# Optimization experiments

Hardware: AMD Instinct MI355X
Metric: run time of the kernel (lower is better)

Reference implementation:

```python
import jax, jax.numpy as jnp
import numpy as np

N_OR = 8          # orientations of the SE(2) discretization
BN_EPS = 1e-5


def _rotate_kernel(W, theta):
    """Rotate a spatial kernel [..., k, k] about its center by theta.
    Bilinear interpolation, zeros outside the kernel support."""
    k = W.shape[-1]
    c = (k - 1) / 2.0
    ys, xs = jnp.meshgrid(jnp.arange(k, dtype=jnp.float32) - c,
                          jnp.arange(k, dtype=jnp.float32) - c, indexing="ij")
    cos, sin = jnp.cos(theta), jnp.sin(theta)
    sy = cos * ys - sin * xs + c   # source coords: rotate sample grid by -theta
    sx = sin * ys + cos * xs + c
    y0 = jnp.floor(sy).astype(jnp.int32)
    x0 = jnp.floor(sx).astype(jnp.int32)
    wy = (sy - y0).astype(W.dtype)
    wx = (sx - x0).astype(W.dtype)

    def gather(yi, xi):
        valid = ((yi >= 0) & (yi < k) & (xi >= 0) & (xi < k)).astype(W.dtype)
        yc = jnp.clip(yi, 0, k - 1)
        xc = jnp.clip(xi, 0, k - 1)
        return W[..., yc, xc] * valid

    return (gather(y0, x0) * (1 - wy) * (1 - wx)
            + gather(y0, x0 + 1) * (1 - wy) * wx
            + gather(y0 + 1, x0) * wy * (1 - wx)
            + gather(y0 + 1, x0 + 1) * wy * wx)


def _thetas():
    return 2.0 * jnp.pi * jnp.arange(N_OR, dtype=jnp.float32) / N_OR


def _lift(x, W):
    """LiftM2Cartesian. x: [B,Cin,H,W] (pre-padded), W: [Cout,Cin,k,k].
    Returns [B,Cout,8,H',W']."""
    Wr = jax.vmap(lambda t: _rotate_kernel(W, t))(_thetas())  # [8,Cout,Cin,k,k]
    co = W.shape[0]
    Wf = Wr.reshape((N_OR * co,) + W.shape[1:])
    y = jax.lax.conv_general_dilated(x, Wf, (1, 1), "VALID",
                                     dimension_numbers=("NCHW", "OIHW", "NCHW"))
    B, _, H, Wd = y.shape
    return y.reshape(B, N_OR, co, H, Wd).transpose(0, 2, 1, 3, 4)


def _gconv(x, K):
    """ConvM2Cartesian. x: [B,Cin,8,H,W] (spatially pre-padded),
    K: [Cout,Cin,8,k,k]. Output orientation m uses the kernel spatially
    rotated by theta_m with the orientation axis cyclically shifted by m."""
    cout, cin, _, k, _ = K.shape
    # orient_idx[m, o] = (o - m) mod 8
    orient_idx = (jnp.arange(N_OR)[None, :] - jnp.arange(N_OR)[:, None]) % N_OR
    Kshift = jnp.moveaxis(K[:, :, orient_idx], 2, 0)        # [8m,Cout,Cin,8o,k,k]
    Km = jax.vmap(_rotate_kernel)(Kshift, _thetas())         # [8m,Cout,Cin,8o,k,k]
    Kf = Km.reshape(N_OR * cout, cin * N_OR, k, k)
    B, _, _, H, Wd = x.shape
    xf = x.reshape(B, cin * N_OR, H, Wd)
    y = jax.lax.conv_general_dilated(xf, Kf, (1, 1), "VALID",
                                     dimension_numbers=("NCHW", "OIHW", "NCHW"))
    Ho, Wo = y.shape[-2:]
    return y.reshape(B, N_OR, cout, Ho, Wo).transpose(0, 2, 1, 3, 4)


def _bn3d(x, gamma, beta):
    """BatchNorm3d (training-mode batch statistics). x: [B,C,O,H,W]."""
    mean = jnp.mean(x, axis=(0, 2, 3, 4), keepdims=True)
    var = jnp.mean((x - mean) ** 2, axis=(0, 2, 3, 4), keepdims=True)
    g = gamma.reshape(1, -1, 1, 1, 1)
    b = beta.reshape(1, -1, 1, 1, 1)
    return g * (x - mean) * jax.lax.rsqrt(var + BN_EPS) + b


def _pad_m2(x, p):
    return jnp.pad(x, ((0, 0), (0, 0), (0, 0), (p, p), (p, p)), mode="reflect")


def setup_inputs() -> dict:
    key = jax.random.key(0)
    ks = jax.random.split(key, 8)
    c = 16
    cin = 3
    x = jax.random.normal(ks[0], (2, cin, 256, 256), dtype=jnp.float32)
    lift_w = jax.random.normal(ks[1], (c, cin, 7, 7), dtype=jnp.float32) / np.sqrt(cin * 49)
    w1 = jax.random.normal(ks[2], (c, c, N_OR, 5, 5), dtype=jnp.float32) / np.sqrt(c * N_OR * 25)
    w2 = jax.random.normal(ks[3], (c, c, N_OR, 5, 5), dtype=jnp.float32) / np.sqrt(c * N_OR * 25)
    w3 = jax.random.normal(ks[4], (c, c, N_OR, 5, 5), dtype=jnp.float32) / np.sqrt(c * N_OR * 25)
    w4 = jax.random.normal(ks[5], (c, c, N_OR, 1, 1), dtype=jnp.float32) / np.sqrt(c * N_OR)
    final_w = jax.random.normal(ks[6], (1, c), dtype=jnp.float32) / np.sqrt(c)
    ones = jnp.ones((c,), dtype=jnp.float32)
    zeros = jnp.zeros((c,), dtype=jnp.float32)
    return {"x": x, "lift_w": lift_w, "w1": w1, "w2": w2, "w3": w3, "w4": w4,
            "final_w": final_w,
            "g0": ones, "b0": zeros, "g1": ones, "b1": zeros, "g2": ones,
            "b2": zeros, "g3": ones, "b3": zeros, "g4": ones, "b4": zeros}


def reference(x, lift_w, w1, w2, w3, w4, final_w,
              g0, b0, g1, b1, g2, b2, g3, b3, g4, b4):
    # lift: ReflectionPad2d(3) -> LiftM2Cartesian(7) -> BN3d -> ReLU
    xp = jnp.pad(x, ((0, 0), (0, 0), (3, 3), (3, 3)), mode="reflect")
    h = jax.nn.relu(_bn3d(_lift(xp, lift_w), g0, b0))          # [B,16,8,H,W]
    # conv1..3: ReflectionPadM2(2) -> ConvM2Cartesian(5) -> BN3d -> ReLU (Dropout3d is identity in eval)
    h = jax.nn.relu(_bn3d(_gconv(_pad_m2(h, 2), w1), g1, b1))
    h = jax.nn.relu(_bn3d(_gconv(_pad_m2(h, 2), w2), g2, b2))
    h = jax.nn.relu(_bn3d(_gconv(_pad_m2(h, 2), w3), g3, b3))
    # conv4: 1x1 group conv -> BN3d -> ReLU
    h = jax.nn.relu(_bn3d(_gconv(h, w4), g4, b4))
    # MaxProjectM2: max over orientation axis
    h = jnp.max(h, axis=2)                                     # [B,16,H,W]
    # final 1x1 conv (no bias) + sigmoid
    return jax.nn.sigmoid(jnp.einsum("bchw,oc->bohw", h, final_w))
```

## Files before the change

kernel.cpp:

```cpp
#include <hip/hip_runtime.h>
#include <hip/hip_bf16.h>
#include <math.h>

#define HW 65536
#define WID 256
#define NOR 8
#define PLANE_C (NOR * HW)
#define PLANE_B (16 * NOR * HW)
#define BN_N 1048576.0f
#define NHWC_STRIDE 136

typedef __attribute__((ext_vector_type(8)))  short  short8;
typedef __attribute__((ext_vector_type(4)))  short  short4v;
typedef __attribute__((ext_vector_type(16))) float  float16;
typedef __attribute__((ext_vector_type(4)))  float  float4v;

__device__ __forceinline__ float b2f(short s) {
    union { unsigned int u; float f; } c;
    c.u = ((unsigned int)(unsigned short)s) << 16;
    return c.f;
}
__device__ __forceinline__ short f2b(float f) {
    union { __hip_bfloat16 h; short s; } c;
    c.h = __float2bfloat16(f);
    return c.s;
}

__global__ void detect_k(const void* __restrict__ x, int* __restrict__ flag) {
    __shared__ int bad;
    if (threadIdx.x == 0) bad = 0;
    __syncthreads();
    const __hip_bfloat16* p = (const __hip_bfloat16*)x;
    for (int i = threadIdx.x; i < 4096; i += 256) {
        float v = __bfloat162float(p[i]);
        if (!(fabsf(v) < 1e4f)) atomicOr(&bad, 1);
    }
    __syncthreads();
    if (threadIdx.x == 0) *flag = bad ? 0 : 1;
}

#define CVT_TOTAL 551392
__global__ void cvt_all_k(const void* p0, const void* p1, const void* p2, const void* p3,
                          const void* p4, const void* p5, const void* p6, const void* p7,
                          const void* p8, const void* p9, const void* p10, const void* p11,
                          const void* p12, const void* p13, const void* p14, const void* p15,
                          const void* p16, float* __restrict__ dst, const int* __restrict__ flag) {
    int i = blockIdx.x * 512 + threadIdx.x;
    if (i >= CVT_TOTAL) return;
    const void* src; int off;
    if      (i < 393216) { src = p0;  off = 0; }
    else if (i < 395568) { src = p1;  off = 393216; }
    else if (i < 446768) { src = p2;  off = 395568; }
    else if (i < 497968) { src = p3;  off = 446768; }
    else if (i < 549168) { src = p4;  off = 497968; }
    else if (i < 551216) { src = p5;  off = 549168; }
    else if (i < 551232) { src = p6;  off = 551216; }
    else if (i < 551248) { src = p7;  off = 551232; }
    else if (i < 551264) { src = p8;  off = 551248; }
    else if (i < 551280) { src = p9;  off = 551264; }
    else if (i < 551296) { src = p10; off = 551280; }
    else if (i < 551312) { src = p11; off = 551296; }
    else if (i < 551328) { src = p12; off = 551312; }
    else if (i < 551344) { src = p13; off = 551328; }
    else if (i < 551360) { src = p14; off = 551344; }
    else if (i < 551376) { src = p15; off = 551360; }
    else                 { src = p16; off = 551376; }
    int j = i - off;
    dst[i] = (*flag) ? __bfloat162float(((const __hip_bfloat16*)src)[j])
                     : ((const float*)src)[j];
}

__device__ float rot_sample(const float* __restrict__ W, int k, float theta, int i, int j) {
    float c = 0.5f * (float)(k - 1);
    float ys = (float)i - c, xs = (float)j - c;
    float cs = cosf(theta), sn = sinf(theta);
    float sy = cs * ys - sn * xs + c;
    float sx = sn * ys + cs * xs + c;
    float fy = floorf(sy), fx = floorf(sx);
    int y0 = (int)fy, x0 = (int)fx;
    float wy = sy - fy, wx = sx - fx;
    float v00 = (y0 >= 0 && y0 < k && x0 >= 0 && x0 < k)                 ? W[y0 * k + x0]           : 0.f;
    float v01 = (y0 >= 0 && y0 < k && x0 + 1 >= 0 && x0 + 1 < k)         ? W[y0 * k + x0 + 1]       : 0.f;
    float v10 = (y0 + 1 >= 0 && y0 + 1 < k && x0 >= 0 && x0 < k)         ? W[(y0 + 1) * k + x0]     : 0.f;
    float v11 = (y0 + 1 >= 0 && y0 + 1 < k && x0 + 1 >= 0 && x0 + 1 < k) ? W[(y0 + 1) * k + x0 + 1] : 0.f;
    return v00 * (1 - wy) * (1 - wx) + v01 * (1 - wy) * wx
         + v10 * wy * (1 - wx) + v11 * wy * wx;
}

__device__ __forceinline__ float theta_of(int m) {
    return (6.2831855f * (float)m) / 8.0f;
}

__device__ __forceinline__ int mirror(int i) {
    i = i < 0 ? -i : i;
    return i >= WID ? (2 * WID - 2 - i) : i;
}

__global__ void pack_blift_k(const float* __restrict__ lw, __hip_bfloat16* __restrict__ B,
                             float* __restrict__ stats) {
    int idx = blockIdx.x * 256 + threadIdx.x;
    if (idx < 32) stats[idx] = 0.f;
    if (idx >= 128 * 160) return;
    int n = idx / 160, k = idx % 160;
    float v = 0.f;
    if (k < 147) {
        int c = n >> 3, o = n & 7;
        int ci = k / 49, s = k % 49;
        v = rot_sample(lw + (c * 3 + ci) * 49, 7, theta_of(o), s / 7, s % 7);
    }
    B[idx] = __float2bfloat16(v);
}

__global__ void pack_bg_k(const float* __restrict__ w, __hip_bfloat16* __restrict__ Bg,
                          float* __restrict__ stats) {
    int idx = blockIdx.x * 256 + threadIdx.x;
    if (idx < 32) stats[idx] = 0.f;
    if (idx >= 409600) return;
    int j = idx & 7;
    int n = (idx >> 3) & 127;
    int kc4 = (idx >> 10) & 3;
    int sq = idx >> 12;
    int s = sq % 25, q = sq / 25;
    int ch = q * 32 + kc4 * 8 + j;
    int co = n >> 3, m = n & 7, ci = ch >> 3, o = ch & 7;
    int oo = (o - m + 8) & 7;
    float v = rot_sample(w + ((co * 16 + ci) * 8 + oo) * 25, 5, theta_of(m), s / 5, s % 5);
    Bg[idx] = __float2bfloat16(v);
}

__global__ void pack_b1_k(const float* __restrict__ w4, __hip_bfloat16* __restrict__ B1,
                          float* __restrict__ stats) {
    int idx = blockIdx.x * 256 + threadIdx.x;
    if (idx < 32) stats[idx] = 0.f;
    if (idx >= 128 * 128) return;
    int n = idx >> 7, ch = idx & 127;
    int co = n >> 3, m = n & 7, ci = ch >> 3, o = ch & 7;
    B1[idx] = __float2bfloat16(w4[(co * 16 + ci) * 8 + ((o - m + 8) & 7)]);
}

__global__ void im2col_lift_k(const float* __restrict__ xb, __hip_bfloat16* __restrict__ A) {
    int idx = blockIdx.x * 256 + threadIdx.x;
    if (idx >= HW * 160) return;
    int px = idx / 160, k = idx % 160;
    float v = 0.f;
    if (k < 147) {
        int ci = k / 49, s = k % 49;
        int gy = mirror((px >> 8) + s / 7 - 3);
        int gx = mirror((px & 255) + s % 7 - 3);
        v = xb[ci * HW + gy * WID + gx];
    }
    A[idx] = __float2bfloat16(v);
}

__device__ __forceinline__ void stats_reduce8(const float16* acc, int lane, int l31,
                                              float* sred) {
#pragma unroll
    for (int nt = 0; nt < 4; nt++) {
        float sv = 0.f, s2v = 0.f;
#pragma unroll
        for (int g = 0; g < 2; g++)
#pragma unroll
            for (int r = 0; r < 16; r++) {
                float v = acc[g * 4 + nt][r];
                sv += v;
                s2v += v * v;
            }
#pragma unroll
        for (int off = 1; off <= 4; off <<= 1) {
            sv += __shfl_xor(sv, off);
            s2v += __shfl_xor(s2v, off);
        }
        sv += __shfl_xor(sv, 32);
        s2v += __shfl_xor(s2v, 32);
        if ((lane & 39) == 0) {
            int c = nt * 4 + (l31 >> 3);
            atomicAdd(&sred[c], sv);
            atomicAdd(&sred[16 + c], s2v);
        }
    }
}

__global__ __launch_bounds__(256, 2) void lift_gemm_k(const __hip_bfloat16* __restrict__ Ah,
                                                      const __hip_bfloat16* __restrict__ Bh,
                                                      __hip_bfloat16* __restrict__ nh_out,
                                                      float* __restrict__ stats) {
    __shared__ short tb[32768];
    __shared__ float sred[32];
    const short* A = (const short*)Ah;
    const short* B = (const short*)Bh;
    int tid = threadIdx.x;
    if (tid < 32) sred[tid] = 0.f;
    int wave = tid >> 6, lane = tid & 63;
    int l31 = lane & 31, half = lane >> 5;
    int p0 = blockIdx.x * 256 + wave * 64;
    float16 acc[8];
#pragma unroll
    for (int i = 0; i < 8; i++) acc[i] = (float16)0.f;
    const short* a0p = A + (size_t)(p0 + l31) * 160 + half * 8;
    const short* a1p = a0p + 32 * 160;
    const short* bp  = B + (size_t)l31 * 160 + half * 8;
#pragma unroll
    for (int ks = 0; ks < 10; ks++) {
        short8 a0 = *(const short8*)(a0p + ks * 16);
        short8 a1 = *(const short8*)(a1p + ks * 16);
#pragma unroll
        for (int nt = 0; nt < 4; nt++) {
            short8 bb = *(const short8*)(bp + nt * 32 * 160 + ks * 16);
            acc[nt]     = __builtin_amdgcn_mfma_f32_32x32x16_bf16(a0, bb, acc[nt], 0, 0, 0);
            acc[4 + nt] = __builtin_amdgcn_mfma_f32_32x32x16_bf16(a1, bb, acc[4 + nt], 0, 0, 0);
        }
    }
#pragma unroll
    for (int g = 0; g < 2; g++)
#pragma unroll
        for (int nt = 0; nt < 4; nt++) {
            int ch = nt * 32 + l31;
#pragma unroll
            for (int r4 = 0; r4 < 4; r4++) {
                int pxb = wave * 64 + g * 32 + 8 * r4 + 4 * half;
#pragma unroll
                for (int i = 0; i < 4; i++)
                    tb[(pxb + i) * 128 + ch] = f2b(acc[g * 4 + nt][r4 * 4 + i]);
            }
        }
    __syncthreads();
    short* outp = (short*)nh_out;
    int pbase = blockIdx.x * 256;
    for (int i = tid; i < 4096; i += 256) {
        int pxl = i >> 4, seg = i & 15;
        *(short8*)(outp + (size_t)(pbase + pxl) * NHWC_STRIDE + seg * 8) =
            *(const short8*)&tb[pxl * 128 + seg * 8];
    }
    stats_reduce8(acc, lane, l31, sred);
    __syncthreads();
    if (tid < 16) {
        atomicAdd(&stats[tid * 2], sred[tid]);
        atomicAdd(&stats[tid * 2 + 1], sred[16 + tid]);
    }
}

__global__ __launch_bounds__(256, 3) void gconv_mfma_k(const __hip_bfloat16* __restrict__ nh_in,
                                                       const __hip_bfloat16* __restrict__ Bgh,
                                                       __hip_bfloat16* __restrict__ nh_out,
                                                       const float* __restrict__ statsPrev,
                                                       const float* __restrict__ gPrev,
                                                       const float* __restrict__ bPrev,
                                                       float* __restrict__ statsNew) {
    __shared__ short Au[16384];
    __shared__ float ssl[32];
    __shared__ float sred[32];
    const short* nhwc = (const short*)nh_in;
    const short* Bg = (const short*)Bgh;
    int bid = blockIdx.x;
    int xcd = bid & 7, q2 = bid >> 3;
    int nhalf = q2 & 1, qt = q2 >> 1;
    int b = xcd >> 2, band = xcd & 3;
    int tx0 = (qt & 15) << 4;
    int ty0 = (band << 6) + ((qt >> 4) << 4);
    int tid = threadIdx.x;
    if (tid < 32) sred[tid] = 0.f;
    if (tid < 16) {
        float mean = statsPrev[tid * 2] / BN_N;
        float var = statsPrev[tid * 2 + 1] / BN_N - mean * mean;
        float sc = gPrev[tid] * rsqrtf(var + 1e-5f);
        ssl[tid * 2] = sc;
        ssl[tid * 2 + 1] = bPrev[tid] - mean * sc;
    }
    int w = tid >> 6, lane = tid & 63;
    int l15 = lane & 15, l4 = lane >> 4;
    float4v acc[16];
#pragma unroll
    for (int i = 0; i < 16; i++) acc[i] = (float4v)0.f;
    const size_t bbase = (size_t)b * HW;
    const int nb = nhalf << 6;

    for (int q = 0; q < 4; q++) {
        __syncthreads();
        for (int i = tid; i < 1600; i += 256) {
            int kc = i / 400, p = i - kc * 400;
            int yl = p / 20, xl = p - yl * 20;
            int gy = mirror(ty0 - 2 + yl);
            int gx = mirror(tx0 - 2 + xl);
            short8 raw = *(const short8*)(nhwc + (bbase + gy * WID + gx) * NHWC_STRIDE
                                          + q * 32 + kc * 8);
            int c = q * 4 + kc;
            float sc = ssl[c * 2], sh = ssl[c * 2 + 1];
            short8 ov;
#pragma unroll
            for (int e = 0; e < 8; e++)
                ov[e] = f2b(fmaxf(fmaf(b2f(raw[e]), sc, sh), 0.f));
            *(short8*)&Au[(kc * 441 + yl * 21 + xl) * 8] = ov;
        }
        __syncthreads();
        for (int s = 0; s < 25; s++) {
            int dy = s / 5 - 2, dx = s % 5 - 2;
            int abase = l4 * 441 + ((w << 2) + 2 + dy) * 21 + (l15 + 2 + dx);
            const short* brow = Bg + ((size_t)(((q * 25 + s) << 2) + l4) * 128 + nb + l15) * 8;
            short8 a0 = *(const short8*)&Au[abase * 8];
            short8 a1 = *(const short8*)&Au[(abase + 21) * 8];
            short8 a2 = *(const short8*)&Au[(abase + 42) * 8];
            short8 a3 = *(const short8*)&Au[(abase + 63) * 8];
#pragma unroll
            for (int nt = 0; nt < 4; nt++) {
                short8 bb = *(const short8*)(brow + nt * 128);
                acc[nt]      = __builtin_amdgcn_mfma_f32_16x16x32_bf16(a0, bb, acc[nt], 0, 0, 0);
                acc[4 + nt]  = __builtin_amdgcn_mfma_f32_16x16x32_bf16(a1, bb, acc[4 + nt], 0, 0, 0);
                acc[8 + nt]  = __builtin_amdgcn_mfma_f32_16x16x32_bf16(a2, bb, acc[8 + nt], 0, 0, 0);
                acc[12 + nt] = __builtin_amdgcn_mfma_f32_16x16x32_bf16(a3, bb, acc[12 + nt], 0, 0, 0);
            }
        }
    }

    __syncthreads();
#pragma unroll
    for (int ag = 0; ag < 4; ag++) {
        int pxb = ((w << 2) + ag) * 16 + (l4 << 2);
#pragma unroll
        for (int nt = 0; nt < 4; nt++) {
            int nl = nt * 16 + l15;
#pragma unroll
            for (int r = 0; r < 4; r++)
                Au[(pxb + r) * 64 + nl] = f2b(acc[ag * 4 + nt][r]);
        }
    }
    __syncthreads();
    short* outp = (short*)nh_out;
    for (int i = tid; i < 2048; i += 256) {
        int pxl = i >> 3, seg = i & 7;
        int y = ty0 + (pxl >> 4), x = tx0 + (pxl & 15);
        *(short8*)(outp + (bbase + y * WID + x) * NHWC_STRIDE + nb + seg * 8) =
            *(const short8*)&Au[pxl * 64 + seg * 8];
    }
#pragma unroll
    for (int nt = 0; nt < 4; nt++) {
        float sv = 0.f, s2v = 0.f;
#pragma unroll
        for (int ag = 0; ag < 4; ag++)
#pragma unroll
            for (int r = 0; r < 4; r++) {
                float v = acc[ag * 4 + nt][r];
                sv += v;
                s2v += v * v;
            }
#pragma unroll
        for (int off = 1; off <= 4; off <<= 1) {
            sv += __shfl_xor(sv, off);
            s2v += __shfl_xor(s2v, off);
        }
        sv += __shfl_xor(sv, 16);
        s2v += __shfl_xor(s2v, 16);
        sv += __shfl_xor(sv, 32);
        s2v += __shfl_xor(s2v, 32);
        if ((lane & 7) == 0 && l4 == 0) {
            int c = (nhalf << 3) + (nt << 1) + (l15 >> 3);
            atomicAdd(&sred[c], sv);
            atomicAdd(&sred[16 + c], s2v);
        }
    }
    __syncthreads();
    if (tid < 16) {
        atomicAdd(&statsNew[tid * 2], sred[tid]);
        atomicAdd(&statsNew[tid * 2 + 1], sred[16 + tid]);
    }
}

__global__ __launch_bounds__(256, 2) void conv1x1_gemm_k(const __hip_bfloat16* __restrict__ nh,
                                                         const __hip_bfloat16* __restrict__ B1h,
                                                         __hip_bfloat16* __restrict__ outP,
                                                         const float* __restrict__ statsPrev,
                                                         const float* __restrict__ gPrev,
                                                         const float* __restrict__ bPrev,
                                                         float* __restrict__ statsNew) {
    __shared__ float sred[32];
    __shared__ float ssl[32];
    const short* nhwc = (const short*)nh;
    const short* B1 = (const short*)B1h;
    int tid = threadIdx.x;
    if (tid < 32) sred[tid] = 0.f;
    if (tid < 16) {
        float mean = statsPrev[tid * 2] / BN_N;
        float var = statsPrev[tid * 2 + 1] / BN_N - mean * mean;
        float sc = gPrev[tid] * rsqrtf(var + 1e-5f);
        ssl[tid * 2] = sc;
        ssl[tid * 2 + 1] = bPrev[tid] - mean * sc;
    }
    __syncthreads();
    int b = blockIdx.y;
    int wave = tid >> 6, lane = tid & 63;
    int l31 = lane & 31, half = lane >> 5;
    int p0 = blockIdx.x * 256 + wave * 64;
    float16 acc[8];
#pragma unroll
    for (int i = 0; i < 8; i++) acc[i] = (float16)0.f;
    const short* a0p = nhwc + ((size_t)b * HW + p0 + l31) * NHWC_STRIDE + half * 8;
    const short* a1p = a0p + 32 * NHWC_STRIDE;
    const short* bp  = B1 + (size_t)l31 * 128 + half * 8;
#pragma unroll
    for (int ks = 0; ks < 8; ks++) {
        short8 r0 = *(const short8*)(a0p + ks * 16);
        short8 r1 = *(const short8*)(a1p + ks * 16);
        int c = ks * 2 + half;
        float sc = ssl[c * 2], sh = ssl[c * 2 + 1];
        short8 a0, a1;
#pragma unroll
        for (int e = 0; e < 8; e++) {
            a0[e] = f2b(fmaxf(fmaf(b2f(r0[e]), sc, sh), 0.f));
            a1[e] = f2b(fmaxf(fmaf(b2f(r1[e]), sc, sh), 0.f));
        }
#pragma unroll
        for (int nt = 0; nt < 4; nt++) {
            short8 bb = *(const short8*)(bp + nt * 32 * 128 + ks * 16);
            acc[nt]     = __builtin_amdgcn_mfma_f32_32x32x16_bf16(a0, bb, acc[nt], 0, 0, 0);
            acc[4 + nt] = __builtin_amdgcn_mfma_f32_32x32x16_bf16(a1, bb, acc[4 + nt], 0, 0, 0);
        }
    }
    short* outb = (short*)outP + (size_t)b * PLANE_B;
#pragma unroll
    for (int g = 0; g < 2; g++)
#pragma unroll
        for (int nt = 0; nt < 4; nt++) {
            int n = nt * 32 + l31;
#pragma unroll
            for (int r4 = 0; r4 < 4; r4++) {
                int base = 8 * r4 + 4 * half;
                short4v v;
                v[0] = f2b(acc[g * 4 + nt][r4 * 4 + 0]);
                v[1] = f2b(acc[g * 4 + nt][r4 * 4 + 1]);
                v[2] = f2b(acc[g * 4 + nt][r4 * 4 + 2]);
                v[3] = f2b(acc[g * 4 + nt][r4 * 4 + 3]);
                *(short4v*)(outb + (size_t)n * HW + p0 + g * 32 + base) = v;
            }
        }
    stats_reduce8(acc, lane, l31, sred);
    __syncthreads();
    if (tid < 16) {
        atomicAdd(&statsNew[tid * 2], sred[tid]);
        atomicAdd(&statsNew[tid * 2 + 1], sred[16 + tid]);
    }
}

__global__ void final_k(const __hip_bfloat16* __restrict__ inP, const float* __restrict__ stats,
                        const float* __restrict__ g, const float* __restrict__ beta,
                        const float* __restrict__ fw, void* __restrict__ out,
                        const int* __restrict__ flag) {
    __shared__ float ssl[32];
    if (threadIdx.x < 16) {
        int c = threadIdx.x;
        float mean = stats[c * 2] / BN_N;
        float var = stats[c * 2 + 1] / BN_N - mean * mean;
        float sc = g[c] * rsqrtf(var + 1e-5f);
        ssl[c * 2] = sc;
        ssl[c * 2 + 1] = beta[c] - mean * sc;
    }
    __syncthreads();
    int i = blockIdx.x * blockDim.x + threadIdx.x;
    int b = i >> 16, pix = i & 65535;
    const short* inp = (const short*)inP;
    float acc = 0.f;
#pragma unroll
    for (int co = 0; co < 16; co++) {
        float sc = ssl[co * 2], sh = ssl[co * 2 + 1];
        float mx = 0.f;
        const short* p = inp + (size_t)b * PLANE_B + (size_t)co * PLANE_C + pix;
#pragma unroll
        for (int m = 0; m < 8; m++) mx = fmaxf(mx, fmaf(b2f(p[m * HW]), sc, sh));
        acc = fmaf(fw[co], mx, acc);
    }
    float r = 1.f / (1.f + expf(-acc));
    if (*flag)
        ((__hip_bfloat16*)out)[i] = __float2bfloat16(r);
    else
        ((float*)out)[i] = r;
}

extern "C" void kernel_launch(void* const* d_in, const int* in_sizes, int n_in,
                              void* d_out, int out_size, void* d_ws, size_t ws_size,
                              hipStream_t stream) {
    float* ws = (float*)d_ws;
    __hip_bfloat16* planarB = (__hip_bfloat16*)ws;
    __hip_bfloat16* nhwcA = (__hip_bfloat16*)(ws + 8388608);
    __hip_bfloat16* nhwcB = (__hip_bfloat16*)(ws + 17301504);
    __hip_bfloat16* Alift = nhwcB;
    __hip_bfloat16* Bg    = (__hip_bfloat16*)(ws + 26214400);
    __hip_bfloat16* Blift = (__hip_bfloat16*)(ws + 26419200);
    __hip_bfloat16* B1    = (__hip_bfloat16*)(ws + 26429440);
    float* xF  = ws + 26437632;
    float* lwF = xF + 393216;
    float* w1F = lwF + 2352;
    float* w2F = w1F + 51200;
    float* w3F = w2F + 51200;
    float* w4F = w3F + 51200;
    float* fwF = w4F + 2048;
    float* gbF = fwF + 16;
    float* statsL = ws + 26989024;
    int*   flag   = (int*)(statsL + 160);

    detect_k<<<1, 256, 0, stream>>>(d_in[0], flag);
    cvt_all_k<<<(CVT_TOTAL + 511) / 512, 512, 0, stream>>>(
        d_in[0], d_in[1], d_in[2], d_in[3], d_in[4], d_in[5], d_in[6], d_in[7], d_in[8],
        d_in[9], d_in[10], d_in[11], d_in[12], d_in[13], d_in[14], d_in[15], d_in[16],
        xF, flag);

    pack_blift_k<<<(128 * 160 + 255) / 256, 256, 0, stream>>>(lwF, Blift, statsL);
    for (int b = 0; b < 2; b++) {
        im2col_lift_k<<<(HW * 160 + 255) / 256, 256, 0, stream>>>(xF + (size_t)b * 3 * HW, Alift);
        lift_gemm_k<<<256, 256, 0, stream>>>(
            Alift, Blift,
            (__hip_bfloat16*)((short*)nhwcA + (size_t)b * HW * NHWC_STRIDE), statsL);
    }

    float* wlist[3] = {w1F, w2F, w3F};
    __hip_bfloat16* nio[4] = {nhwcA, nhwcB, nhwcA, nhwcB};
    for (int l = 0; l < 3; l++) {
        pack_bg_k<<<(409600 + 255) / 256, 256, 0, stream>>>(wlist[l], Bg, statsL + 32 * (l + 1));
        gconv_mfma_k<<<1024, 256, 0, stream>>>(nio[l], Bg, nio[l + 1],
                                               statsL + 32 * l, gbF + 32 * l, gbF + 32 * l + 16,
                                               statsL + 32 * (l + 1));
    }

    pack_b1_k<<<(128 * 128 + 255) / 256, 256, 0, stream>>>(w4F, B1, statsL + 128);
    conv1x1_gemm_k<<<dim3(256, 2), 256, 0, stream>>>(nio[3], B1, planarB,
                                                     statsL + 96, gbF + 96, gbF + 112,
                                                     statsL + 128);

    final_k<<<(2 * HW) / 256, 256, 0, stream>>>(planarB, statsL + 128, gbF + 128, gbF + 144,
                                                fwF, d_out, flag);
}
```

Measured before the change: 557.9 us.

## Fuse lift im2col into GEMM and merge weight packing into one kernel

Weight packing for the lift layer, all three group-conv layers and the 1x1 layer now runs in a single kernel into separate buffers, and it zeroes all stats slots at once. This replaces six small launches with one. The lift im2col is done inside the GEMM: each block stages a reflected 22x22x3 input tile in shared memory and builds the bf16 A fragments on the fly, so the 160-wide im2col matrix is no longer written to or read from global memory. Both batches are covered by a single 2D grid. In exchange, the GEMM inner loop now does scalar LDS gathers and conversions, and the lift output is written in 16x16 spatial tiles rather than contiguous pixel rows.

```diff
diff --git a/kernel.cpp b/kernel.cpp
--- a/kernel.cpp
+++ b/kernel.cpp
@@ -96,60 +96,53 @@
     return i >= WID ? (2 * WID - 2 - i) : i;
 }
 
-__global__ void pack_blift_k(const float* __restrict__ lw, __hip_bfloat16* __restrict__ B,
-                             float* __restrict__ stats) {
+#define PK_BLIFT 20480
+#define PK_BG 409600
+#define PK_TOTAL (PK_BLIFT + 3 * PK_BG + 16384)
+__global__ void mega_pack_k(const float* __restrict__ lwF, const float* __restrict__ w1F,
+                            const float* __restrict__ w2F, const float* __restrict__ w3F,
+                            const float* __restrict__ w4F,
+                            __hip_bfloat16* __restrict__ Blift, __hip_bfloat16* __restrict__ Bg1,
+                            __hip_bfloat16* __restrict__ Bg2, __hip_bfloat16* __restrict__ Bg3,
+                            __hip_bfloat16* __restrict__ B1, float* __restrict__ statsL) {
     int idx = blockIdx.x * 256 + threadIdx.x;
-    if (idx < 32) stats[idx] = 0.f;
-    if (idx >= 128 * 160) return;
-    int n = idx / 160, k = idx % 160;
-    float v = 0.f;
-    if (k < 147) {
-        int c = n >> 3, o = n & 7;
-        int ci = k / 49, s = k % 49;
-        v = rot_sample(lw + (c * 3 + ci) * 49, 7, theta_of(o), s / 7, s % 7);
-    }
-    B[idx] = __float2bfloat16(v);
-}
-
-__global__ void pack_bg_k(const float* __restrict__ w, __hip_bfloat16* __restrict__ Bg,
-                          float* __restrict__ stats) {
-    int idx = blockIdx.x * 256 + threadIdx.x;
-    if (idx < 32) stats[idx] = 0.f;
-    if (idx >= 409600) return;
-    int j = idx & 7;
-    int n = (idx >> 3) & 127;
-    int kc4 = (idx >> 10) & 3;
-    int sq = idx >> 12;
-    int s = sq % 25, q = sq / 25;
-    int ch = q * 32 + kc4 * 8 + j;
-    int co = n >> 3, m = n & 7, ci = ch >> 3, o = ch & 7;
-    int oo = (o - m + 8) & 7;
-    float v = rot_sample(w + ((co * 16 + ci) * 8 + oo) * 25, 5, theta_of(m), s / 5, s % 5);
-    Bg[idx] = __float2bfloat16(v);
-}
-
-__global__ void pack_b1_k(const float* __restrict__ w4, __hip_bfloat16* __restrict__ B1,
-                          float* __restrict__ stats) {
-    int idx = blockIdx.x * 256 + threadIdx.x;
-    if (idx < 32) stats[idx] = 0.f;
-    if (idx >= 128 * 128) return;
-    int n = idx >> 7, ch = idx & 127;
-    int co = n >> 3, m = n & 7, ci = ch >> 3, o = ch & 7;
-    B1[idx] = __float2bfloat16(w4[(co * 16 + ci) * 8 + ((o - m + 8) & 7)]);
-}
-
-__global__ void im2col_lift_k(const float* __restrict__ xb, __hip_bfloat16* __restrict__ A) {
-    int idx = blockIdx.x * 256 + threadIdx.x;
-    if (idx >= HW * 160) return;
-    int px = idx / 160, k = idx % 160;
-    float v = 0.f;
-    if (k < 147) {
-        int ci = k / 49, s = k % 49;
-        int gy = mirror((px >> 8) + s / 7 - 3);
-        int gx = mirror((px & 255) + s % 7 - 3);
-        v = xb[ci * HW + gy * WID + gx];
-    }
-    A[idx] = __float2bfloat16(v);
+    if (idx < 160) statsL[idx] = 0.f;
+    if (idx >= PK_TOTAL) return;
+    if (idx < PK_BLIFT) {
+        int n = idx / 160, k = idx % 160;
+        float v = 0.f;
+        if (k < 147) {
+            int c = n >> 3, o = n & 7;
+            int ci = k / 49, s = k % 49;
+            v = rot_sample(lwF + (c * 3 + ci) * 49, 7, theta_of(o), s / 7, s % 7);
+        }
+        Blift[idx] = __float2bfloat16(v);
+        return;
+    }
+    idx -= PK_BLIFT;
+    if (idx < 3 * PK_BG) {
+        int l = idx / PK_BG;
+        int r = idx - l * PK_BG;
+        const float* w = (l == 0) ? w1F : ((l == 1) ? w2F : w3F);
+        __hip_bfloat16* Bg = (l == 0) ? Bg1 : ((l == 1) ? Bg2 : Bg3);
+        int j = r & 7;
+        int n = (r >> 3) & 127;
+        int kc4 = (r >> 10) & 3;
+        int sq = r >> 12;
+        int s = sq % 25, q = sq / 25;
+        int ch = q * 32 + kc4 * 8 + j;
+        int co = n >> 3, m = n & 7, ci = ch >> 3, o = ch & 7;
+        int oo = (o - m + 8) & 7;
+        Bg[r] = __float2bfloat16(
+            rot_sample(w + ((co * 16 + ci) * 8 + oo) * 25, 5, theta_of(m), s / 5, s % 5));
+        return;
+    }
+    idx -= 3 * PK_BG;
+    {
+        int n = idx >> 7, ch = idx & 127;
+        int co = n >> 3, m = n & 7, ci = ch >> 3, o = ch & 7;
+        B1[idx] = __float2bfloat16(w4F[(co * 16 + ci) * 8 + ((o - m + 8) & 7)]);
+    }
 }
 
 __device__ __forceinline__ void stats_reduce8(const float16* acc, int lane, int l31,
@@ -180,29 +173,52 @@
     }
 }
 
-__global__ __launch_bounds__(256, 2) void lift_gemm_k(const __hip_bfloat16* __restrict__ Ah,
-                                                      const __hip_bfloat16* __restrict__ Bh,
-                                                      __hip_bfloat16* __restrict__ nh_out,
-                                                      float* __restrict__ stats) {
+__global__ __launch_bounds__(256, 2) void lift_fused_k(const float* __restrict__ xF,
+                                                       const __hip_bfloat16* __restrict__ Bh,
+                                                       __hip_bfloat16* __restrict__ nh_out,
+                                                       float* __restrict__ stats) {
+    __shared__ float Xs[3 * 484];
     __shared__ short tb[32768];
     __shared__ float sred[32];
-    const short* A = (const short*)Ah;
     const short* B = (const short*)Bh;
     int tid = threadIdx.x;
     if (tid < 32) sred[tid] = 0.f;
+    int tile = blockIdx.x;
+    int b = blockIdx.y;
+    int tx0 = (tile & 15) << 4, ty0 = (tile >> 4) << 4;
+    for (int i = tid; i < 1452; i += 256) {
+        int ci = i / 484, p = i - ci * 484;
+        int yl = p / 22, xl = p - yl * 22;
+        int gy = mirror(ty0 - 3 + yl), gx = mirror(tx0 - 3 + xl);
+        Xs[i] = xF[((size_t)b * 3 + ci) * HW + gy * WID + gx];
+    }
+    __syncthreads();
     int wave = tid >> 6, lane = tid & 63;
     int l31 = lane & 31, half = lane >> 5;
-    int p0 = blockIdx.x * 256 + wave * 64;
     float16 acc[8];
 #pragma unroll
     for (int i = 0; i < 8; i++) acc[i] = (float16)0.f;
-    const short* a0p = A + (size_t)(p0 + l31) * 160 + half * 8;
-    const short* a1p = a0p + 32 * 160;
-    const short* bp  = B + (size_t)l31 * 160 + half * 8;
+    int pxl0 = wave * 64 + l31;
+    int py0 = pxl0 >> 4, px0 = pxl0 & 15;
+    int py1 = (pxl0 + 32) >> 4, px1 = (pxl0 + 32) & 15;
+    const short* bp = B + (size_t)l31 * 160 + half * 8;
 #pragma unroll
     for (int ks = 0; ks < 10; ks++) {
-        short8 a0 = *(const short8*)(a0p + ks * 16);
-        short8 a1 = *(const short8*)(a1p + ks * 16);
+        short8 a0, a1;
+#pragma unroll
+        for (int j = 0; j < 8; j++) {
+            int k = ks * 16 + half * 8 + j;
+            float v0 = 0.f, v1 = 0.f;
+            if (k < 147) {
+                int ci = (k < 49) ? 0 : ((k < 98) ? 1 : 2);
+                int s = k - ci * 49;
+                int sy = s / 7, sx = s - sy * 7;
+                v0 = Xs[ci * 484 + (py0 + sy) * 22 + px0 + sx];
+                v1 = Xs[ci * 484 + (py1 + sy) * 22 + px1 + sx];
+            }
+            a0[j] = f2b(v0);
+            a1[j] = f2b(v1);
+        }
 #pragma unroll
         for (int nt = 0; nt < 4; nt++) {
             short8 bb = *(const short8*)(bp + nt * 32 * 160 + ks * 16);
@@ -224,11 +240,11 @@
             }
         }
     __syncthreads();
-    short* outp = (short*)nh_out;
-    int pbase = blockIdx.x * 256;
+    short* outp = (short*)nh_out + (size_t)b * HW * NHWC_STRIDE;
     for (int i = tid; i < 4096; i += 256) {
         int pxl = i >> 4, seg = i & 15;
-        *(short8*)(outp + (size_t)(pbase + pxl) * NHWC_STRIDE + seg * 8) =
+        int y = ty0 + (pxl >> 4), x = tx0 + (pxl & 15);
+        *(short8*)(outp + ((size_t)y * WID + x) * NHWC_STRIDE + seg * 8) =
             *(const short8*)&tb[pxl * 128 + seg * 8];
     }
     stats_reduce8(acc, lane, l31, sred);
@@ -480,11 +496,12 @@
     __hip_bfloat16* planarB = (__hip_bfloat16*)ws;
     __hip_bfloat16* nhwcA = (__hip_bfloat16*)(ws + 8388608);
     __hip_bfloat16* nhwcB = (__hip_bfloat16*)(ws + 17301504);
-    __hip_bfloat16* Alift = nhwcB;
-    __hip_bfloat16* Bg    = (__hip_bfloat16*)(ws + 26214400);
-    __hip_bfloat16* Blift = (__hip_bfloat16*)(ws + 26419200);
-    __hip_bfloat16* B1    = (__hip_bfloat16*)(ws + 26429440);
-    float* xF  = ws + 26437632;
+    __hip_bfloat16* Bg1   = (__hip_bfloat16*)(ws + 26214400);
+    __hip_bfloat16* Bg2   = (__hip_bfloat16*)(ws + 26419200);
+    __hip_bfloat16* Bg3   = (__hip_bfloat16*)(ws + 26624000);
+    __hip_bfloat16* Blift = (__hip_bfloat16*)(ws + 26828800);
+    __hip_bfloat16* B1    = (__hip_bfloat16*)(ws + 26839040);
+    float* xF  = ws + 26847232;
     float* lwF = xF + 393216;
     float* w1F = lwF + 2352;
     float* w2F = w1F + 51200;
@@ -492,7 +509,7 @@
     float* w4F = w3F + 51200;
     float* fwF = w4F + 2048;
     float* gbF = fwF + 16;
-    float* statsL = ws + 26989024;
+    float* statsL = ws + 27398624;
     int*   flag   = (int*)(statsL + 160);
 
     detect_k<<<1, 256, 0, stream>>>(d_in[0], flag);
@@ -501,24 +518,19 @@
         d_in[9], d_in[10], d_in[11], d_in[12], d_in[13], d_in[14], d_in[15], d_in[16],
         xF, flag);
 
-    pack_blift_k<<<(128 * 160 + 255) / 256, 256, 0, stream>>>(lwF, Blift, statsL);
-    for (int b = 0; b < 2; b++) {
-        im2col_lift_k<<<(HW * 160 + 255) / 256, 256, 0, stream>>>(xF + (size_t)b * 3 * HW, Alift);
-        lift_gemm_k<<<256, 256, 0, stream>>>(
-            Alift, Blift,
-            (__hip_bfloat16*)((short*)nhwcA + (size_t)b * HW * NHWC_STRIDE), statsL);
-    }
-
-    float* wlist[3] = {w1F, w2F, w3F};
+    mega_pack_k<<<(PK_TOTAL + 255) / 256, 256, 0, stream>>>(
+        lwF, w1F, w2F, w3F, w4F, Blift, Bg1, Bg2, Bg3, B1, statsL);
+
+    lift_fused_k<<<dim3(256, 2), 256, 0, stream>>>(xF, Blift, nhwcA, statsL);
+
+    __hip_bfloat16* Bgs[3] = {Bg1, Bg2, Bg3};
     __hip_bfloat16* nio[4] = {nhwcA, nhwcB, nhwcA, nhwcB};
     for (int l = 0; l < 3; l++) {
-        pack_bg_k<<<(409600 + 255) / 256, 256, 0, stream>>>(wlist[l], Bg, statsL + 32 * (l + 1));
-        gconv_mfma_k<<<1024, 256, 0, stream>>>(nio[l], Bg, nio[l + 1],
+        gconv_mfma_k<<<1024, 256, 0, stream>>>(nio[l], Bgs[l], nio[l + 1],
                                                statsL + 32 * l, gbF + 32 * l, gbF + 32 * l + 16,
                                                statsL + 32 * (l + 1));
     }
 
-    pack_b1_k<<<(128 * 128 + 255) / 256, 256, 0, stream>>>(w4F, B1, statsL + 128);
     conv1x1_gemm_k<<<dim3(256, 2), 256, 0, stream>>>(nio[3], B1, planarB,
                                                      statsL + 96, gbF + 96, gbF + 112,
                                                      statsL + 128);
```

New measurement: 502.8 us. 9.9% less time.
